# Kernel tuning notes

Measured on AMD Instinct MI355X. Metric: run time of the kernel, lower is better.

The kernel has to match this reference:

```python
import jax, jax.numpy as jnp
import numpy as np

D_MODEL = 1024
NUM_HEADS = 16
DK = D_MODEL // NUM_HEADS  # 64


def setup_inputs() -> dict:
    key = jax.random.key(0)
    kx, kq, kk, kv, ko = jax.random.split(key, 5)
    B, S = 4, 2048
    # xavier-uniform-ish scale for square [d_model, d_model] matrices
    bound = float(np.sqrt(6.0 / (D_MODEL + D_MODEL)))
    uni = lambda k: jax.random.uniform(k, (D_MODEL, D_MODEL), jnp.float32, -bound, bound)
    return {
        "x": jax.random.normal(kx, (B, S, D_MODEL), jnp.float32),
        "q_heads": uni(kq),
        "k_heads": uni(kk),
        "v_heads": uni(kv),
        "output_proj": uni(ko),
    }


def reference(x, q_heads, k_heads, v_heads, output_proj):
    B, S, _ = x.shape
    # projections: x @ W.T, split into heads -> [B, H, S, dk]
    def proj(W):
        return (x @ W.T).reshape(B, S, NUM_HEADS, DK).transpose(0, 2, 1, 3)
    q, k, v = proj(q_heads), proj(k_heads), proj(v_heads)
    scale = 1.0 / jnp.sqrt(jnp.asarray(DK, x.dtype))
    scores = jnp.einsum("bhqd,bhkd->bhqk", q, k) * scale  # [B,H,S,S]
    causal = jnp.triu(jnp.ones((S, S), bool), k=1)
    scores = jnp.where(causal, jnp.asarray(-jnp.inf, scores.dtype), scores)
    attn = jax.nn.softmax(scores, axis=-1)
    out = jnp.einsum("bhqk,bhkd->bhqd", attn, v)  # [B,H,S,dk]
    out = out.transpose(0, 2, 1, 3).reshape(B, S, D_MODEL)
    return out @ output_proj.T
```

## Files before the change

kernel.cpp:

```cpp
#include <hip/hip_runtime.h>
#include <hip/hip_bf16.h>

#define AS1 __attribute__((address_space(1)))
#define AS3 __attribute__((address_space(3)))

typedef __hip_bfloat16 bf16;
typedef short bf16x8 __attribute__((ext_vector_type(8)));
typedef float f32x4 __attribute__((ext_vector_type(4)));

static constexpr int D = 1024, S = 2048, NB = 4, NH = 16, DK = 64;
static constexpr int M = NB * S;

__device__ __forceinline__ void gload16(void* lds_dst, const void* gsrc) {
  __builtin_amdgcn_global_load_lds((const AS1 void*)gsrc, (AS3 void*)lds_dst, 16, 0, 0);
}

__global__ void cvt_bf16_kernel(const float* __restrict__ src, bf16* __restrict__ dst, int n) {
  int i = (blockIdx.x * blockDim.x + threadIdx.x) * 4;
  int stride = gridDim.x * blockDim.x * 4;
  for (; i < n; i += stride) {
    float4 v = *(const float4*)(src + i);
    union { bf16 h[4]; uint2 u; } t;
    t.h[0] = __float2bfloat16(v.x);
    t.h[1] = __float2bfloat16(v.y);
    t.h[2] = __float2bfloat16(v.z);
    t.h[3] = __float2bfloat16(v.w);
    *(uint2*)(dst + i) = t.u;
  }
}

template <int MODE>
__global__ __launch_bounds__(256)
void gemm_bt(const bf16* __restrict__ A, const bf16* __restrict__ Bw,
             void* __restrict__ out, int K, int ldc, float scale) {
  __shared__ __align__(16) char lds[32768];
  char* Asm = lds;
  char* Bsm = lds + 16384;
  const int tid = threadIdx.x;
  const int w = tid >> 6, l = tid & 63;
  const int ql = l & 15, g = l >> 4;
  const int rowA = blockIdx.x * 128;
  const int rowB = blockIdx.y * 128;
  const int wr = (w >> 1) * 64, wc = (w & 1) * 64;

  f32x4 acc[4][4] = {};

  for (int k0 = 0; k0 < K; k0 += 64) {
#pragma unroll
    for (int i = 0; i < 4; ++i) {
      int o = ((i * 4 + w) << 10) + (l << 4);
      int row = o >> 7;
      int u = ((o >> 4) & 7) ^ (row & 7);
      gload16(Asm + ((i * 4 + w) << 10), A + (size_t)(rowA + row) * K + k0 + (u << 3));
      gload16(Bsm + ((i * 4 + w) << 10), Bw + (size_t)(rowB + row) * K + k0 + (u << 3));
    }
    __syncthreads();
#pragma unroll
    for (int kk = 0; kk < 2; ++kk) {
      bf16x8 af[4], bfr[4];
#pragma unroll
      for (int m = 0; m < 4; ++m) {
        int row = wr + m * 16 + ql;
        int sub = ((kk << 2) + g) ^ (row & 7);
        af[m] = *(const bf16x8*)(Asm + row * 128 + sub * 16);
      }
#pragma unroll
      for (int n = 0; n < 4; ++n) {
        int row = wc + n * 16 + ql;
        int sub = ((kk << 2) + g) ^ (row & 7);
        bfr[n] = *(const bf16x8*)(Bsm + row * 128 + sub * 16);
      }
#pragma unroll
      for (int m = 0; m < 4; ++m)
#pragma unroll
        for (int n = 0; n < 4; ++n)
          acc[m][n] = __builtin_amdgcn_mfma_f32_16x16x32_bf16(af[m], bfr[n], acc[m][n], 0, 0, 0);
    }
    __syncthreads();
  }

#pragma unroll
  for (int m = 0; m < 4; ++m)
#pragma unroll
    for (int n = 0; n < 4; ++n)
#pragma unroll
      for (int r = 0; r < 4; ++r) {
        int gm = rowA + wr + m * 16 + g * 4 + r;
        int gn = rowB + wc + n * 16 + ql;
        float v = acc[m][n][r] * scale;
        if (MODE == 0) {
          int b = gm >> 11, s = gm & 2047, h = gn >> 6, d = gn & 63;
          ((bf16*)out)[(((size_t)(b * 16 + h) * S) + s) * DK + d] = __float2bfloat16(v);
        } else if (MODE == 1) {
          int b = gn >> 11, s = gn & 2047;
          ((bf16*)out)[((size_t)b * 1024 + gm) * S + s] = __float2bfloat16(v);
        } else {
          ((float*)out)[(size_t)gm * ldc + gn] = v;
        }
      }
}

__global__ __launch_bounds__(256)
void attn_kernel(const bf16* __restrict__ Q, const bf16* __restrict__ Km,
                 const bf16* __restrict__ Vt, bf16* __restrict__ O) {
  __shared__ __align__(16) char P[4][2][2048];
  const int tid = threadIdx.x;
  const int w = tid >> 6, l = tid & 63;
  const int ql = l & 15, g = l >> 4;
  const int bh = blockIdx.y;
  const int sidx = blockIdx.x + 16 * w;
  const int qbase = sidx * 32;
  const int swz = (ql & 7) << 4;
  const float L2E = 1.44269504f;
  const float THR = 8.0f;

  const bf16* Qb = Q + (size_t)bh * S * DK;
  const bf16* Kb = Km + (size_t)bh * S * DK;
  const bf16* Vb = Vt + (size_t)bh * DK * S;

  bf16x8 qf[2][2];
#pragma unroll
  for (int sub = 0; sub < 2; ++sub)
#pragma unroll
    for (int kk = 0; kk < 2; ++kk)
      qf[sub][kk] = *(const bf16x8*)(Qb + (size_t)(qbase + sub * 16 + ql) * DK + kk * 32 + g * 8);

  f32x4 oacc[2][4] = {};
  float mrow[2] = {-3e38f, -3e38f};
  float lrow[2] = {0.f, 0.f};

  const int kv_end = qbase + 32;
  for (int kv0 = 0; kv0 < kv_end; kv0 += 64) {
    const bool last = (kv0 + 64 >= kv_end);

    f32x4 st[2][4];
#pragma unroll
    for (int sub = 0; sub < 2; ++sub)
#pragma unroll
      for (int mt = 0; mt < 4; ++mt) st[sub][mt] = f32x4{0.f, 0.f, 0.f, 0.f};
    __builtin_amdgcn_s_setprio(1);
#pragma unroll
    for (int kk = 0; kk < 2; ++kk) {
      bf16x8 kf[4];
#pragma unroll
      for (int mt = 0; mt < 4; ++mt)
        kf[mt] = *(const bf16x8*)(Kb + (size_t)(kv0 + mt * 16 + ql) * DK + kk * 32 + g * 8);
#pragma unroll
      for (int sub = 0; sub < 2; ++sub)
#pragma unroll
        for (int mt = 0; mt < 4; ++mt)
          st[sub][mt] = __builtin_amdgcn_mfma_f32_16x16x32_bf16(kf[mt], qf[sub][kk], st[sub][mt], 0, 0, 0);
    }
    __builtin_amdgcn_s_setprio(0);

    bf16x8 vf[2][4];
#pragma unroll
    for (int kk = 0; kk < 2; ++kk)
#pragma unroll
      for (int n = 0; n < 4; ++n)
        vf[kk][n] = *(const bf16x8*)(Vb + (size_t)(n * 16 + ql) * S + kv0 + kk * 32 + g * 8);

#pragma unroll
    for (int sub = 0; sub < 2; ++sub) {
      const int qpos = qbase + sub * 16 + ql;
      if (last) {
#pragma unroll
        for (int mt = 0; mt < 4; ++mt)
#pragma unroll
          for (int r = 0; r < 4; ++r) {
            int kvpos = kv0 + mt * 16 + g * 4 + r;
            if (kvpos > qpos) st[sub][mt][r] = -3e38f;
          }
      }
      float tmax = st[sub][0][0];
#pragma unroll
      for (int mt = 0; mt < 4; ++mt)
#pragma unroll
        for (int r = 0; r < 4; ++r) tmax = fmaxf(tmax, st[sub][mt][r]);
      if (__any(tmax > mrow[sub] + THR)) {
        float rm = tmax;
        rm = fmaxf(rm, __shfl_xor(rm, 16, 64));
        rm = fmaxf(rm, __shfl_xor(rm, 32, 64));
        float mnew = fmaxf(mrow[sub], rm);
        float sc = exp2f((mrow[sub] - mnew) * L2E);
        mrow[sub] = mnew;
        lrow[sub] *= sc;
#pragma unroll
        for (int r = 0; r < 4; ++r) {
          float scr = __shfl(sc, g * 4 + r, 16);
#pragma unroll
          for (int n = 0; n < 4; ++n) oacc[sub][n][r] *= scr;
        }
      }

      float psum = 0.f;
#pragma unroll
      for (int mt = 0; mt < 4; ++mt) {
        union { ushort us[4]; uint2 u; } pk;
#pragma unroll
        for (int r = 0; r < 4; ++r) {
          float p = exp2f((st[sub][mt][r] - mrow[sub]) * L2E);
          psum += p;
          union { bf16 b; ushort u; } cv;
          cv.b = __float2bfloat16(p);
          pk.us[r] = cv.u;
        }
        *(uint2*)&P[w][sub][((ql << 7) + (mt << 5) + (g << 3)) ^ swz] = pk.u;
      }
      lrow[sub] += psum;
    }

    __builtin_amdgcn_s_setprio(1);
#pragma unroll
    for (int kk = 0; kk < 2; ++kk)
#pragma unroll
      for (int sub = 0; sub < 2; ++sub) {
        bf16x8 pa = *(const bf16x8*)&P[w][sub][((ql << 7) + (kk << 6) + (g << 4)) ^ swz];
#pragma unroll
        for (int n = 0; n < 4; ++n)
          oacc[sub][n] = __builtin_amdgcn_mfma_f32_16x16x32_bf16(pa, vf[kk][n], oacc[sub][n], 0, 0, 0);
      }
    __builtin_amdgcn_s_setprio(0);
  }

  const int bo = bh >> 4, hh = bh & 15;
  bf16* Ob = O + (size_t)bo * S * D + hh * 64;
#pragma unroll
  for (int sub = 0; sub < 2; ++sub) {
    float lr = lrow[sub];
    lr += __shfl_xor(lr, 16, 64);
    lr += __shfl_xor(lr, 32, 64);
    float ldv[4];
#pragma unroll
    for (int r = 0; r < 4; ++r) ldv[r] = __shfl(lr, g * 4 + r, 16);
#pragma unroll
    for (int r = 0; r < 4; ++r) {
      int qpos = qbase + sub * 16 + g * 4 + r;
      float inv = 1.f / ldv[r];
#pragma unroll
      for (int n = 0; n < 4; ++n)
        Ob[(size_t)qpos * D + n * 16 + ql] = __float2bfloat16(oacc[sub][n][r] * inv);
    }
  }
}

extern "C" void kernel_launch(void* const* d_in, const int* in_sizes, int n_in,
                              void* d_out, int out_size, void* d_ws, size_t ws_size,
                              hipStream_t stream) {
  const float* x  = (const float*)d_in[0];
  const float* wq = (const float*)d_in[1];
  const float* wk = (const float*)d_in[2];
  const float* wv = (const float*)d_in[3];
  const float* wo = (const float*)d_in[4];

  char* ws = (char*)d_ws;
  bf16* xb  = (bf16*)(ws);
  bf16* wqb = (bf16*)(ws + (16u << 20));
  bf16* wkb = (bf16*)(ws + (18u << 20));
  bf16* wvb = (bf16*)(ws + (20u << 20));
  bf16* wob = (bf16*)(ws + (22u << 20));
  bf16* Qb  = (bf16*)(ws + (24u << 20));
  bf16* Kb  = (bf16*)(ws + (40u << 20));
  bf16* Vtb = (bf16*)(ws + (56u << 20));
  bf16* Ob  = (bf16*)(ws + (72u << 20));

  cvt_bf16_kernel<<<2048, 256, 0, stream>>>(x, xb, M * D);
  cvt_bf16_kernel<<<1024, 256, 0, stream>>>(wq, wqb, D * D);
  cvt_bf16_kernel<<<1024, 256, 0, stream>>>(wk, wkb, D * D);
  cvt_bf16_kernel<<<1024, 256, 0, stream>>>(wv, wvb, D * D);
  cvt_bf16_kernel<<<1024, 256, 0, stream>>>(wo, wob, D * D);

  gemm_bt<0><<<dim3(M / 128, D / 128), 256, 0, stream>>>(xb, wqb, Qb, D, D, 0.125f);
  gemm_bt<0><<<dim3(M / 128, D / 128), 256, 0, stream>>>(xb, wkb, Kb, D, D, 1.0f);
  gemm_bt<1><<<dim3(D / 128, M / 128), 256, 0, stream>>>(wvb, xb, Vtb, D, D, 1.0f);

  attn_kernel<<<dim3(16, NB * NH), 256, 0, stream>>>(Qb, Kb, Vtb, Ob);

  gemm_bt<2><<<dim3(M / 128, D / 128), 256, 0, stream>>>(Ob, wob, d_out, D, D, 1.0f);
}
```

Baseline: 277.8 us.

## Balance causal attention work by pairing mirrored 16-row query tiles per wave

Each wave now handles two 16-row query tiles, j and 127-j, one after the other, instead of a single 32-row tile. This evens out the causal triangle's work across waves, where before the waves on late tiles ran much longer. The grid is flattened to 1D with a remap that groups 8 heads together, which may improve L2 reuse. Launch bounds now request 4 blocks per SM to raise occupancy. In exchange, each K/V load now feeds only 16 query rows instead of 32, so K/V traffic and MFMA reuse per load get worse.

After: 350.6 us. +26.2%, slower.

```diff
diff --git a/kernel.cpp b/kernel.cpp
--- a/kernel.cpp
+++ b/kernel.cpp
@@ -100,16 +100,17 @@
       }
 }
 
-__global__ __launch_bounds__(256)
+__global__ __launch_bounds__(256, 4)
 void attn_kernel(const bf16* __restrict__ Q, const bf16* __restrict__ Km,
                  const bf16* __restrict__ Vt, bf16* __restrict__ O) {
-  __shared__ __align__(16) char P[4][2][2048];
+  __shared__ __align__(16) char P[4][2048];
   const int tid = threadIdx.x;
   const int w = tid >> 6, l = tid & 63;
   const int ql = l & 15, g = l >> 4;
-  const int bh = blockIdx.y;
-  const int sidx = blockIdx.x + 16 * w;
-  const int qbase = sidx * 32;
+  const int id = blockIdx.x;
+  const int bh = (id & 7) + 8 * (id >> 7);
+  const int x = (id >> 3) & 15;
+  const int pair = x + 16 * w;
   const int swz = (ql & 7) << 4;
   const float L2E = 1.44269504f;
   const float THR = 8.0f;
@@ -117,79 +118,77 @@
   const bf16* Qb = Q + (size_t)bh * S * DK;
   const bf16* Kb = Km + (size_t)bh * S * DK;
   const bf16* Vb = Vt + (size_t)bh * DK * S;
-
-  bf16x8 qf[2][2];
-#pragma unroll
-  for (int sub = 0; sub < 2; ++sub)
+  const int bo = bh >> 4, hh = bh & 15;
+  bf16* Ob = O + (size_t)bo * S * D + hh * 64;
+
+#pragma unroll
+  for (int s2 = 0; s2 < 2; ++s2) {
+    const int j = (s2 == 0) ? pair : 127 - pair;
+    const int qbase = j << 4;
+    const int qpos = qbase + ql;
+
+    bf16x8 qf[2];
 #pragma unroll
     for (int kk = 0; kk < 2; ++kk)
-      qf[sub][kk] = *(const bf16x8*)(Qb + (size_t)(qbase + sub * 16 + ql) * DK + kk * 32 + g * 8);
-
-  f32x4 oacc[2][4] = {};
-  float mrow[2] = {-3e38f, -3e38f};
-  float lrow[2] = {0.f, 0.f};
-
-  const int kv_end = qbase + 32;
-  for (int kv0 = 0; kv0 < kv_end; kv0 += 64) {
-    const bool last = (kv0 + 64 >= kv_end);
-
-    f32x4 st[2][4];
-#pragma unroll
-    for (int sub = 0; sub < 2; ++sub)
-#pragma unroll
-      for (int mt = 0; mt < 4; ++mt) st[sub][mt] = f32x4{0.f, 0.f, 0.f, 0.f};
-    __builtin_amdgcn_s_setprio(1);
-#pragma unroll
-    for (int kk = 0; kk < 2; ++kk) {
-      bf16x8 kf[4];
-#pragma unroll
-      for (int mt = 0; mt < 4; ++mt)
-        kf[mt] = *(const bf16x8*)(Kb + (size_t)(kv0 + mt * 16 + ql) * DK + kk * 32 + g * 8);
-#pragma unroll
-      for (int sub = 0; sub < 2; ++sub)
+      qf[kk] = *(const bf16x8*)(Qb + (size_t)(qbase + ql) * DK + kk * 32 + g * 8);
+
+    f32x4 oacc[4] = {};
+    float mrow = -3e38f;
+    float lrow = 0.f;
+
+    const int kv_end = qbase + 16;
+    for (int kv0 = 0; kv0 < kv_end; kv0 += 64) {
+      const bool last = (kv0 + 64 >= kv_end);
+
+      f32x4 st[4] = {};
+      __builtin_amdgcn_s_setprio(1);
+#pragma unroll
+      for (int kk = 0; kk < 2; ++kk) {
+        bf16x8 kf[4];
 #pragma unroll
         for (int mt = 0; mt < 4; ++mt)
-          st[sub][mt] = __builtin_amdgcn_mfma_f32_16x16x32_bf16(kf[mt], qf[sub][kk], st[sub][mt], 0, 0, 0);
-    }
-    __builtin_amdgcn_s_setprio(0);
-
-    bf16x8 vf[2][4];
-#pragma unroll
-    for (int kk = 0; kk < 2; ++kk)
-#pragma unroll
-      for (int n = 0; n < 4; ++n)
-        vf[kk][n] = *(const bf16x8*)(Vb + (size_t)(n * 16 + ql) * S + kv0 + kk * 32 + g * 8);
-
-#pragma unroll
-    for (int sub = 0; sub < 2; ++sub) {
-      const int qpos = qbase + sub * 16 + ql;
+          kf[mt] = *(const bf16x8*)(Kb + (size_t)(kv0 + mt * 16 + ql) * DK + kk * 32 + g * 8);
+#pragma unroll
+        for (int mt = 0; mt < 4; ++mt)
+          st[mt] = __builtin_amdgcn_mfma_f32_16x16x32_bf16(kf[mt], qf[kk], st[mt], 0, 0, 0);
+      }
+      __builtin_amdgcn_s_setprio(0);
+
+      bf16x8 vf[2][4];
+#pragma unroll
+      for (int kk = 0; kk < 2; ++kk)
+#pragma unroll
+        for (int n = 0; n < 4; ++n)
+          vf[kk][n] = *(const bf16x8*)(Vb + (size_t)(n * 16 + ql) * S + kv0 + kk * 32 + g * 8);
+
       if (last) {
 #pragma unroll
         for (int mt = 0; mt < 4; ++mt)
 #pragma unroll
           for (int r = 0; r < 4; ++r) {
             int kvpos = kv0 + mt * 16 + g * 4 + r;
-            if (kvpos > qpos) st[sub][mt][r] = -3e38f;
+            if (kvpos > qpos) st[mt][r] = -3e38f;
           }
       }
-      float tmax = st[sub][0][0];
+
+      float tmax = st[0][0];
 #pragma unroll
       for (int mt = 0; mt < 4; ++mt)
 #pragma unroll
-        for (int r = 0; r < 4; ++r) tmax = fmaxf(tmax, st[sub][mt][r]);
-      if (__any(tmax > mrow[sub] + THR)) {
+        for (int r = 0; r < 4; ++r) tmax = fmaxf(tmax, st[mt][r]);
+      if (__any(tmax > mrow + THR)) {
         float rm = tmax;
         rm = fmaxf(rm, __shfl_xor(rm, 16, 64));
         rm = fmaxf(rm, __shfl_xor(rm, 32, 64));
-        float mnew = fmaxf(mrow[sub], rm);
-        float sc = exp2f((mrow[sub] - mnew) * L2E);
-        mrow[sub] = mnew;
-        lrow[sub] *= sc;
+        float mnew = fmaxf(mrow, rm);
+        float sc = exp2f((mrow - mnew) * L2E);
+        mrow = mnew;
+        lrow *= sc;
 #pragma unroll
         for (int r = 0; r < 4; ++r) {
           float scr = __shfl(sc, g * 4 + r, 16);
 #pragma unroll
-          for (int n = 0; n < 4; ++n) oacc[sub][n][r] *= scr;
+          for (int n = 0; n < 4; ++n) oacc[n][r] *= scr;
         }
       }
 
@@ -199,35 +198,28 @@
         union { ushort us[4]; uint2 u; } pk;
 #pragma unroll
         for (int r = 0; r < 4; ++r) {
-          float p = exp2f((st[sub][mt][r] - mrow[sub]) * L2E);
+          float p = exp2f((st[mt][r] - mrow) * L2E);
           psum += p;
           union { bf16 b; ushort u; } cv;
           cv.b = __float2bfloat16(p);
           pk.us[r] = cv.u;
         }
-        *(uint2*)&P[w][sub][((ql << 7) + (mt << 5) + (g << 3)) ^ swz] = pk.u;
-      }
-      lrow[sub] += psum;
-    }
-
-    __builtin_amdgcn_s_setprio(1);
-#pragma unroll
-    for (int kk = 0; kk < 2; ++kk)
-#pragma unroll
-      for (int sub = 0; sub < 2; ++sub) {
-        bf16x8 pa = *(const bf16x8*)&P[w][sub][((ql << 7) + (kk << 6) + (g << 4)) ^ swz];
+        *(uint2*)&P[w][((ql << 7) + (mt << 5) + (g << 3)) ^ swz] = pk.u;
+      }
+      lrow += psum;
+
+      __builtin_amdgcn_s_setprio(1);
+#pragma unroll
+      for (int kk = 0; kk < 2; ++kk) {
+        bf16x8 pa = *(const bf16x8*)&P[w][((ql << 7) + (kk << 6) + (g << 4)) ^ swz];
 #pragma unroll
         for (int n = 0; n < 4; ++n)
-          oacc[sub][n] = __builtin_amdgcn_mfma_f32_16x16x32_bf16(pa, vf[kk][n], oacc[sub][n], 0, 0, 0);
-      }
-    __builtin_amdgcn_s_setprio(0);
-  }
-
-  const int bo = bh >> 4, hh = bh & 15;
-  bf16* Ob = O + (size_t)bo * S * D + hh * 64;
-#pragma unroll
-  for (int sub = 0; sub < 2; ++sub) {
-    float lr = lrow[sub];
+          oacc[n] = __builtin_amdgcn_mfma_f32_16x16x32_bf16(pa, vf[kk][n], oacc[n], 0, 0, 0);
+      }
+      __builtin_amdgcn_s_setprio(0);
+    }
+
+    float lr = lrow;
     lr += __shfl_xor(lr, 16, 64);
     lr += __shfl_xor(lr, 32, 64);
     float ldv[4];
@@ -235,11 +227,11 @@
     for (int r = 0; r < 4; ++r) ldv[r] = __shfl(lr, g * 4 + r, 16);
 #pragma unroll
     for (int r = 0; r < 4; ++r) {
-      int qpos = qbase + sub * 16 + g * 4 + r;
+      int qrow = qbase + g * 4 + r;
       float inv = 1.f / ldv[r];
 #pragma unroll
       for (int n = 0; n < 4; ++n)
-        Ob[(size_t)qpos * D + n * 16 + ql] = __float2bfloat16(oacc[sub][n][r] * inv);
+        Ob[(size_t)qrow * D + n * 16 + ql] = __float2bfloat16(oacc[n][r] * inv);
     }
   }
 }
@@ -274,7 +266,7 @@
   gemm_bt<0><<<dim3(M / 128, D / 128), 256, 0, stream>>>(xb, wkb, Kb, D, D, 1.0f);
   gemm_bt<1><<<dim3(D / 128, M / 128), 256, 0, stream>>>(wvb, xb, Vtb, D, D, 1.0f);
 
-  attn_kernel<<<dim3(16, NB * NH), 256, 0, stream>>>(Qb, Kb, Vtb, Ob);
+  attn_kernel<<<dim3(1024), 256, 0, stream>>>(Qb, Kb, Vtb, Ob);
 
   gemm_bt<2><<<dim3(M / 128, D / 128), 256, 0, stream>>>(Ob, wob, d_out, D, D, 1.0f);
 }
```

## Split KV range across wave pairs and pair causal tiles for balanced attention

Applied to the files above, without the earlier changes.

The attention kernel changes its work split. Each pair of waves now handles one 32-row query tile, and the two waves each take half of its KV range and merge their softmax partials (max, sum, output accumulator) through shared memory. Each block processes two tiles, j and 63-j, so causal work is balanced across blocks. The grid becomes 1D with a bh-interleaved mapping, and launch bounds ask for 4 blocks per SM. This targets the load imbalance and long serial KV loops of late query tiles, at the cost of extra LDS traffic, syncthreads and merge math.

New measurement: 331.3 us. 1.19x slower.

```diff
diff --git a/kernel.cpp b/kernel.cpp
--- a/kernel.cpp
+++ b/kernel.cpp
@@ -100,16 +100,20 @@
       }
 }
 
-__global__ __launch_bounds__(256)
+__global__ __launch_bounds__(256, 4)
 void attn_kernel(const bf16* __restrict__ Q, const bf16* __restrict__ Km,
                  const bf16* __restrict__ Vt, bf16* __restrict__ O) {
   __shared__ __align__(16) char P[4][2][2048];
+  __shared__ float CB[2][64][37];
   const int tid = threadIdx.x;
   const int w = tid >> 6, l = tid & 63;
   const int ql = l & 15, g = l >> 4;
-  const int bh = blockIdx.y;
-  const int sidx = blockIdx.x + 16 * w;
-  const int qbase = sidx * 32;
+  const int id = blockIdx.x;
+  const int bh = (id & 7) + 8 * (id >> 7);
+  const int x = (id >> 3) & 15;
+  const int pi = w >> 1;
+  const int late = w & 1;
+  const int pbase = x + 16 * pi;
   const int swz = (ql & 7) << 4;
   const float L2E = 1.44269504f;
   const float THR = 8.0f;
@@ -117,130 +121,166 @@
   const bf16* Qb = Q + (size_t)bh * S * DK;
   const bf16* Kb = Km + (size_t)bh * S * DK;
   const bf16* Vb = Vt + (size_t)bh * DK * S;
-
-  bf16x8 qf[2][2];
-#pragma unroll
-  for (int sub = 0; sub < 2; ++sub)
-#pragma unroll
-    for (int kk = 0; kk < 2; ++kk)
-      qf[sub][kk] = *(const bf16x8*)(Qb + (size_t)(qbase + sub * 16 + ql) * DK + kk * 32 + g * 8);
-
-  f32x4 oacc[2][4] = {};
-  float mrow[2] = {-3e38f, -3e38f};
-  float lrow[2] = {0.f, 0.f};
-
-  const int kv_end = qbase + 32;
-  for (int kv0 = 0; kv0 < kv_end; kv0 += 64) {
-    const bool last = (kv0 + 64 >= kv_end);
-
-    f32x4 st[2][4];
-#pragma unroll
-    for (int sub = 0; sub < 2; ++sub)
-#pragma unroll
-      for (int mt = 0; mt < 4; ++mt) st[sub][mt] = f32x4{0.f, 0.f, 0.f, 0.f};
-    __builtin_amdgcn_s_setprio(1);
-#pragma unroll
-    for (int kk = 0; kk < 2; ++kk) {
-      bf16x8 kf[4];
-#pragma unroll
-      for (int mt = 0; mt < 4; ++mt)
-        kf[mt] = *(const bf16x8*)(Kb + (size_t)(kv0 + mt * 16 + ql) * DK + kk * 32 + g * 8);
-#pragma unroll
-      for (int sub = 0; sub < 2; ++sub)
-#pragma unroll
-        for (int mt = 0; mt < 4; ++mt)
-          st[sub][mt] = __builtin_amdgcn_mfma_f32_16x16x32_bf16(kf[mt], qf[sub][kk], st[sub][mt], 0, 0, 0);
-    }
-    __builtin_amdgcn_s_setprio(0);
-
-    bf16x8 vf[2][4];
-#pragma unroll
-    for (int kk = 0; kk < 2; ++kk)
-#pragma unroll
-      for (int n = 0; n < 4; ++n)
-        vf[kk][n] = *(const bf16x8*)(Vb + (size_t)(n * 16 + ql) * S + kv0 + kk * 32 + g * 8);
-
-#pragma unroll
-    for (int sub = 0; sub < 2; ++sub) {
-      const int qpos = qbase + sub * 16 + ql;
-      if (last) {
-#pragma unroll
-        for (int mt = 0; mt < 4; ++mt)
-#pragma unroll
-          for (int r = 0; r < 4; ++r) {
-            int kvpos = kv0 + mt * 16 + g * 4 + r;
-            if (kvpos > qpos) st[sub][mt][r] = -3e38f;
-          }
-      }
-      float tmax = st[sub][0][0];
-#pragma unroll
-      for (int mt = 0; mt < 4; ++mt)
-#pragma unroll
-        for (int r = 0; r < 4; ++r) tmax = fmaxf(tmax, st[sub][mt][r]);
-      if (__any(tmax > mrow[sub] + THR)) {
-        float rm = tmax;
-        rm = fmaxf(rm, __shfl_xor(rm, 16, 64));
-        rm = fmaxf(rm, __shfl_xor(rm, 32, 64));
-        float mnew = fmaxf(mrow[sub], rm);
-        float sc = exp2f((mrow[sub] - mnew) * L2E);
-        mrow[sub] = mnew;
-        lrow[sub] *= sc;
-#pragma unroll
-        for (int r = 0; r < 4; ++r) {
-          float scr = __shfl(sc, g * 4 + r, 16);
-#pragma unroll
-          for (int n = 0; n < 4; ++n) oacc[sub][n][r] *= scr;
-        }
-      }
-
-      float psum = 0.f;
-#pragma unroll
-      for (int mt = 0; mt < 4; ++mt) {
-        union { ushort us[4]; uint2 u; } pk;
-#pragma unroll
-        for (int r = 0; r < 4; ++r) {
-          float p = exp2f((st[sub][mt][r] - mrow[sub]) * L2E);
-          psum += p;
-          union { bf16 b; ushort u; } cv;
-          cv.b = __float2bfloat16(p);
-          pk.us[r] = cv.u;
-        }
-        *(uint2*)&P[w][sub][((ql << 7) + (mt << 5) + (g << 3)) ^ swz] = pk.u;
-      }
-      lrow[sub] += psum;
-    }
-
-    __builtin_amdgcn_s_setprio(1);
-#pragma unroll
-    for (int kk = 0; kk < 2; ++kk)
-#pragma unroll
-      for (int sub = 0; sub < 2; ++sub) {
-        bf16x8 pa = *(const bf16x8*)&P[w][sub][((ql << 7) + (kk << 6) + (g << 4)) ^ swz];
-#pragma unroll
-        for (int n = 0; n < 4; ++n)
-          oacc[sub][n] = __builtin_amdgcn_mfma_f32_16x16x32_bf16(pa, vf[kk][n], oacc[sub][n], 0, 0, 0);
-      }
-    __builtin_amdgcn_s_setprio(0);
-  }
-
   const int bo = bh >> 4, hh = bh & 15;
   bf16* Ob = O + (size_t)bo * S * D + hh * 64;
-#pragma unroll
-  for (int sub = 0; sub < 2; ++sub) {
-    float lr = lrow[sub];
-    lr += __shfl_xor(lr, 16, 64);
-    lr += __shfl_xor(lr, 32, 64);
-    float ldv[4];
-#pragma unroll
-    for (int r = 0; r < 4; ++r) ldv[r] = __shfl(lr, g * 4 + r, 16);
-#pragma unroll
-    for (int r = 0; r < 4; ++r) {
-      int qpos = qbase + sub * 16 + g * 4 + r;
-      float inv = 1.f / ldv[r];
-#pragma unroll
-      for (int n = 0; n < 4; ++n)
-        Ob[(size_t)qpos * D + n * 16 + ql] = __float2bfloat16(oacc[sub][n][r] * inv);
-    }
+
+  for (int round = 0; round < 2; ++round) {
+    const int j = (round == 0) ? pbase : 63 - pbase;
+    const int qbase = j << 5;
+    const int T = (qbase + 32 + 63) >> 6;
+    const int TA = T >> 1;
+    const int myLate = late ^ round;
+    const int t0 = myLate ? TA : 0;
+    const int t1 = myLate ? T : TA;
+
+    bf16x8 qf[2][2];
+#pragma unroll
+    for (int sub = 0; sub < 2; ++sub)
+#pragma unroll
+      for (int kk = 0; kk < 2; ++kk)
+        qf[sub][kk] = *(const bf16x8*)(Qb + (size_t)(qbase + sub * 16 + ql) * DK + kk * 32 + g * 8);
+
+    f32x4 oacc[2][4] = {};
+    float mrow[2] = {-3e38f, -3e38f};
+    float lrow[2] = {0.f, 0.f};
+
+    for (int t = t0; t < t1; ++t) {
+      const int kv0 = t << 6;
+      const bool maskT = (t == T - 1);
+
+      f32x4 st[2][4];
+#pragma unroll
+      for (int sub = 0; sub < 2; ++sub)
+#pragma unroll
+        for (int mt = 0; mt < 4; ++mt) st[sub][mt] = f32x4{0.f, 0.f, 0.f, 0.f};
+      __builtin_amdgcn_s_setprio(1);
+#pragma unroll
+      for (int kk = 0; kk < 2; ++kk) {
+        bf16x8 kf[4];
+#pragma unroll
+        for (int mt = 0; mt < 4; ++mt)
+          kf[mt] = *(const bf16x8*)(Kb + (size_t)(kv0 + mt * 16 + ql) * DK + kk * 32 + g * 8);
+#pragma unroll
+        for (int sub = 0; sub < 2; ++sub)
+#pragma unroll
+          for (int mt = 0; mt < 4; ++mt)
+            st[sub][mt] = __builtin_amdgcn_mfma_f32_16x16x32_bf16(kf[mt], qf[sub][kk], st[sub][mt], 0, 0, 0);
+      }
+      __builtin_amdgcn_s_setprio(0);
+
+      bf16x8 vf[2][4];
+#pragma unroll
+      for (int kk = 0; kk < 2; ++kk)
+#pragma unroll
+        for (int n = 0; n < 4; ++n)
+          vf[kk][n] = *(const bf16x8*)(Vb + (size_t)(n * 16 + ql) * S + kv0 + kk * 32 + g * 8);
+
+#pragma unroll
+      for (int sub = 0; sub < 2; ++sub) {
+        const int qpos = qbase + sub * 16 + ql;
+        if (maskT) {
+#pragma unroll
+          for (int mt = 0; mt < 4; ++mt)
+#pragma unroll
+            for (int r = 0; r < 4; ++r) {
+              int kvpos = kv0 + mt * 16 + g * 4 + r;
+              if (kvpos > qpos) st[sub][mt][r] = -3e38f;
+            }
+        }
+        float tmax = st[sub][0][0];
+#pragma unroll
+        for (int mt = 0; mt < 4; ++mt)
+#pragma unroll
+          for (int r = 0; r < 4; ++r) tmax = fmaxf(tmax, st[sub][mt][r]);
+        if (__any(tmax > mrow[sub] + THR)) {
+          float rm = tmax;
+          rm = fmaxf(rm, __shfl_xor(rm, 16, 64));
+          rm = fmaxf(rm, __shfl_xor(rm, 32, 64));
+          float mnew = fmaxf(mrow[sub], rm);
+          float sc = exp2f((mrow[sub] - mnew) * L2E);
+          mrow[sub] = mnew;
+          lrow[sub] *= sc;
+#pragma unroll
+          for (int r = 0; r < 4; ++r) {
+            float scr = __shfl(sc, g * 4 + r, 16);
+#pragma unroll
+            for (int n = 0; n < 4; ++n) oacc[sub][n][r] *= scr;
+          }
+        }
+        float psum = 0.f;
+#pragma unroll
+        for (int mt = 0; mt < 4; ++mt) {
+          union { ushort us[4]; uint2 u; } pk;
+#pragma unroll
+          for (int r = 0; r < 4; ++r) {
+            float p = exp2f((st[sub][mt][r] - mrow[sub]) * L2E);
+            psum += p;
+            union { bf16 b; ushort u; } cv;
+            cv.b = __float2bfloat16(p);
+            pk.us[r] = cv.u;
+          }
+          *(uint2*)&P[w][sub][((ql << 7) + (mt << 5) + (g << 3)) ^ swz] = pk.u;
+        }
+        lrow[sub] += psum;
+      }
+
+      __builtin_amdgcn_s_setprio(1);
+#pragma unroll
+      for (int kk = 0; kk < 2; ++kk)
+#pragma unroll
+        for (int sub = 0; sub < 2; ++sub) {
+          bf16x8 pa = *(const bf16x8*)&P[w][sub][((ql << 7) + (kk << 6) + (g << 4)) ^ swz];
+#pragma unroll
+          for (int n = 0; n < 4; ++n)
+            oacc[sub][n] = __builtin_amdgcn_mfma_f32_16x16x32_bf16(pa, vf[kk][n], oacc[sub][n], 0, 0, 0);
+        }
+      __builtin_amdgcn_s_setprio(0);
+    }
+
+    if (myLate) {
+      float* cb = &CB[pi][l][0];
+      cb[0] = mrow[0]; cb[1] = mrow[1];
+      cb[2] = lrow[0]; cb[3] = lrow[1];
+#pragma unroll
+      for (int sub = 0; sub < 2; ++sub)
+#pragma unroll
+        for (int n = 0; n < 4; ++n)
+#pragma unroll
+          for (int r = 0; r < 4; ++r)
+            cb[4 + sub * 16 + n * 4 + r] = oacc[sub][n][r];
+    }
+    __syncthreads();
+    if (!myLate) {
+      const float* cb = &CB[pi][l][0];
+#pragma unroll
+      for (int sub = 0; sub < 2; ++sub) {
+        float mG = cb[sub], lG = cb[2 + sub];
+        float m = fmaxf(mrow[sub], mG);
+        float fF = exp2f((mrow[sub] - m) * L2E);
+        float fG = exp2f((mG - m) * L2E);
+        float lr = fF * lrow[sub] + fG * lG;
+        lr += __shfl_xor(lr, 16, 64);
+        lr += __shfl_xor(lr, 32, 64);
+        float ldv[4], fFr[4], fGr[4];
+#pragma unroll
+        for (int r = 0; r < 4; ++r) {
+          ldv[r] = __shfl(lr, g * 4 + r, 16);
+          fFr[r] = __shfl(fF, g * 4 + r, 16);
+          fGr[r] = __shfl(fG, g * 4 + r, 16);
+        }
+#pragma unroll
+        for (int r = 0; r < 4; ++r) {
+          int qrow = qbase + sub * 16 + g * 4 + r;
+          float inv = 1.f / ldv[r];
+#pragma unroll
+          for (int n = 0; n < 4; ++n) {
+            float ov = fFr[r] * oacc[sub][n][r] + fGr[r] * cb[4 + sub * 16 + n * 4 + r];
+            Ob[(size_t)qrow * D + n * 16 + ql] = __float2bfloat16(ov * inv);
+          }
+        }
+      }
+    }
+    __syncthreads();
   }
 }
 
@@ -274,7 +314,7 @@
   gemm_bt<0><<<dim3(M / 128, D / 128), 256, 0, stream>>>(xb, wkb, Kb, D, D, 1.0f);
   gemm_bt<1><<<dim3(D / 128, M / 128), 256, 0, stream>>>(wvb, xb, Vtb, D, D, 1.0f);
 
-  attn_kernel<<<dim3(16, NB * NH), 256, 0, stream>>>(Qb, Kb, Vtb, Ob);
+  attn_kernel<<<dim3(1024), 256, 0, stream>>>(Qb, Kb, Vtb, Ob);
 
   gemm_bt<2><<<dim3(M / 128, D / 128), 256, 0, stream>>>(Ob, wob, d_out, D, D, 1.0f);
 }
```
